# Kernel optimization log

Hardware: AMD Instinct MI355X
Metric: run time of the kernel (lower is better)

## Reference

```python
import jax, jax.numpy as jnp
import numpy as np

# --- static config (from init_kwargs) ---
PC_RANGE = np.array([-51.2, -51.2, -5.0, 51.2, 51.2, 3.0], np.float32)
VOXEL_SIZE = np.array([0.2, 0.2, 8.0], np.float32)
GRID = np.round((PC_RANGE[3:] - PC_RANGE[:3]) / VOXEL_SIZE).astype(np.int64)  # [512,512,1]
GX, GY, GZ = int(GRID[0]), int(GRID[1]), int(GRID[2])
GTOT = GX * GY * GZ  # sentinel linear id for invalid points
MAXV = 30000   # max_voxels_num
MAXP = 20      # max_points_in_voxel
NORM_DIMS = np.array([0, 1, 2], np.int32)
B, N, C = 4, 300000, 5


def _voxelize_one(pts):
    """Hard voxelization of one point cloud [N, C] -> (feat [MAXV,MAXP,C], coors [MAXV,3] (zyx), npts [MAXV])."""
    pc_min = jnp.asarray(PC_RANGE[:3], pts.dtype)
    vsize = jnp.asarray(VOXEL_SIZE, pts.dtype)
    coords = jnp.floor((pts[:, :3] - pc_min) / vsize).astype(jnp.int32)  # [N,3] xyz
    grid = jnp.array([GX, GY, GZ], jnp.int32)
    inb = jnp.all((coords >= 0) & (coords < grid), axis=1)
    lin = coords[:, 2] * (GY * GX) + coords[:, 1] * GX + coords[:, 0]
    lin = jnp.where(inb, lin, GTOT)  # invalid points sort to the end
    order = jnp.argsort(lin)  # stable sort -> deterministic assignment
    lin_s, pts_s, coords_s = lin[order], pts[order], coords[order]
    n = pts.shape[0]
    new = jnp.concatenate([jnp.ones((1,), bool), lin_s[1:] != lin_s[:-1]])
    slot = jnp.cumsum(new.astype(jnp.int32)) - 1           # voxel slot (order of first appearance)
    idx = jnp.arange(n, dtype=jnp.int32)
    run_start = jax.lax.cummax(jnp.where(new, idx, 0))     # start index of each voxel run
    rank = idx - run_start                                  # point rank inside its voxel
    keep = (lin_s < GTOT) & (slot < MAXV) & (rank < MAXP)
    slot_s = jnp.where(keep, slot, MAXV)                    # out-of-range -> dropped by scatter
    rank_s = jnp.where(keep, rank, 0)
    feat = jnp.zeros((MAXV, MAXP, pts.shape[1]), pts.dtype).at[slot_s, rank_s].set(pts_s, mode='drop')
    coors = jnp.full((MAXV, 3), -1, jnp.int32).at[slot_s].set(coords_s[:, ::-1], mode='drop')  # zyx
    npts = jnp.zeros((MAXV,), jnp.int32).at[slot_s].add(keep.astype(jnp.int32), mode='drop')
    return feat, coors, npts


def setup_inputs() -> dict:
    key = jax.random.key(0)
    k1, _ = jax.random.split(key)
    u = jax.random.uniform(k1, (B, N, C), dtype=jnp.float32)
    lo = jnp.array([-51.2, -51.2, -5.0, 0.0, 0.0], jnp.float32)
    hi = jnp.array([51.2, 51.2, 3.0, 1.0, 1.0], jnp.float32)
    points = lo + u * (hi - lo)
    norm_range = jnp.asarray(PC_RANGE)
    return {"points": points, "norm_range": norm_range}


def reference(points, norm_range):
    bs = points.shape[0]
    feat, coors, npts = jax.vmap(_voxelize_one)(points)
    feat = feat.reshape(bs * MAXV, MAXP, C)
    npts = npts.reshape(bs * MAXV)
    bidx = jnp.repeat(jnp.arange(bs, dtype=jnp.int32), MAXV)[:, None]
    coors_batch = jnp.concatenate([bidx, coors.reshape(bs * MAXV, 3)], axis=1)  # [B*MAXV, 4]
    # per-dim range normalization: (f - start) / (max - min) on NORM_DIMS only
    dims = jnp.asarray(NORM_DIMS)
    half = norm_range.shape[0] // 2
    start = jnp.zeros((C,), feat.dtype).at[dims].set(norm_range[:half])
    scale = jnp.ones((C,), feat.dtype).at[dims].set(norm_range[half:] - norm_range[:half])
    f = (feat - start) / scale
    # padding-indicator mask
    mask = (jnp.arange(MAXP)[None, :] < npts[:, None]).astype(f.dtype)
    f = f * mask[:, :, None]
    # unsqueeze(0).permute(0, 3, 2, 1) -> [1, C, MAXP, B*MAXV]
    features = jnp.transpose(f[None], (0, 3, 2, 1))
    return features, coors_batch
```

## Files before the change

### kernel.cpp

```cpp
#include <hip/hip_runtime.h>
#include <stdint.h>

typedef unsigned long long u64;
typedef uint32_t u32;
typedef unsigned char u8;

#define B_ 4
#define N_ 300000
#define C_ 5
#define GX_ 512
#define GY_ 512
#define GZ_ 1
#define GTOT_ (GX_*GY_*GZ_)
#define NW_ (GTOT_/64)
#define MAXV_ 30000
#define MAXP_ 20
#define ROWS_ (B_*MAXV_)
#define OUT0_ELEMS_ (C_*MAXP_*ROWS_)

#define OCCF_Q_ (B_*GTOT_/16)
#define CNT2_Q_ (ROWS_/4)
#define INIT_Q_ (OCCF_Q_ + CNT2_Q_)

__device__ __forceinline__ int voxel_lin(float x, float y, float z) {
    float qx = (x + 51.2f) * 5.0f;
    float qy = (y + 51.2f) * 5.0f;
    float qz = (z + 5.0f) * 0.125f;
    int cx = (int)floorf(qx);
    int cy = (int)floorf(qy);
    int cz = (int)floorf(qz);
    if (cx < 0 || cx >= GX_ || cy < 0 || cy >= GY_ || cz < 0 || cz >= GZ_) return -1;
    return (cz * GY_ + cy) * GX_ + cx;
}

__global__ void k_init(uint4* __restrict__ occF4, uint4* __restrict__ cnt2q) {
    int i = blockIdx.x * blockDim.x + threadIdx.x;
    if (i < OCCF_Q_) occF4[i] = make_uint4(0u, 0u, 0u, 0u);
    else if (i < INIT_Q_) cnt2q[i - OCCF_Q_] = make_uint4(0u, 0u, 0u, 0u);
}

__global__ void k_mark(const float* __restrict__ pts, u8* __restrict__ occF,
                       int* __restrict__ linb) {
    int i = blockIdx.x * blockDim.x + threadIdx.x;
    int b = blockIdx.y;
    if (i >= N_) return;
    const float* p = pts + ((size_t)b * N_ + i) * C_;
    int lin = voxel_lin(p[0], p[1], p[2]);
    linb[(size_t)b * N_ + i] = lin;
    if (lin >= 0) occF[(size_t)b * GTOT_ + lin] = (u8)1;
}

__global__ void k_maskcnt(const u8* __restrict__ occF, u64* __restrict__ occ,
                          u32* __restrict__ wordPop) {
    int i = blockIdx.x * blockDim.x + threadIdx.x;
    int b = blockIdx.y;
    u8 f = occF[(size_t)b * GTOT_ + i];
    u64 m = __ballot(f != 0);
    if ((threadIdx.x & 63) == 0) {
        int w = i >> 6;
        occ[(size_t)b * NW_ + w] = m;
        wordPop[(size_t)b * NW_ + w] = (u32)__popcll(m);
    }
}

__global__ __launch_bounds__(1024) void k_scan2(const u32* __restrict__ wordPop,
                                                u32* __restrict__ wordOff,
                                                u32* __restrict__ nOcc) {
    int b = blockIdx.x;
    int t = threadIdx.x;
    const uint4* wp = (const uint4*)(wordPop + (size_t)b * NW_);
    uint4 v = wp[t];
    __shared__ u32 sh[1024];
    sh[t] = v.x + v.y + v.z + v.w;
    __syncthreads();
    for (int off = 1; off < 1024; off <<= 1) {
        u32 u = (t >= off) ? sh[t - off] : 0u;
        __syncthreads();
        sh[t] += u;
        __syncthreads();
    }
    u32 excl = (t > 0) ? sh[t - 1] : 0u;
    u32* wo = wordOff + (size_t)b * NW_ + t * 4;
    wo[0] = excl;
    wo[1] = excl + v.x;
    wo[2] = excl + v.x + v.y;
    wo[3] = excl + v.x + v.y + v.z;
    if (t == 1023) nOcc[b] = sh[1023];
}

__global__ void k_scatter(const int* __restrict__ linb, const u64* __restrict__ occ,
                          const u32* __restrict__ wordOff,
                          u32* __restrict__ cnt2, u32* __restrict__ idxbuf,
                          u32* __restrict__ voxOf) {
    int i = blockIdx.x * blockDim.x + threadIdx.x;
    int b = blockIdx.y;
    if (i >= N_) return;
    int lin = linb[(size_t)b * N_ + i];
    if (lin < 0) return;
    int w = lin >> 6, bit = lin & 63;
    u32 baseOff = wordOff[(size_t)b * NW_ + w];
    if (baseOff >= MAXV_) return;
    u64 m = occ[(size_t)b * NW_ + w];
    u32 slot = baseOff + (u32)__popcll(m & ((1ull << bit) - 1ull));
    if (slot >= MAXV_) return;
    u32 r = atomicAdd(&cnt2[b * MAXV_ + slot], 1u);
    if (r == 0) voxOf[b * MAXV_ + slot] = (u32)lin;
    if (r < MAXP_) idxbuf[((size_t)b * MAXV_ + slot) * MAXP_ + r] = (u32)i;
}

__global__ void k_out(const float* __restrict__ pts, const float* __restrict__ nr,
                      const u32* __restrict__ voxOf, const u32* __restrict__ cnt2,
                      const u32* __restrict__ idxbuf, const u32* __restrict__ nOcc,
                      float* __restrict__ out0, float* __restrict__ out1) {
    int row = blockIdx.x * blockDim.x + threadIdx.x;
    if (row >= ROWS_) return;
    int b = row / MAXV_;
    int local = row - b * MAXV_;
    u32 nv = nOcc[b];
    bool valid = (u32)local < (nv < MAXV_ ? nv : (u32)MAXV_);
    u32 lin = 0;
    int n = 0;
    u32 idxs[MAXP_];
    if (valid) {
        lin = voxOf[row];
        n = (int)min(cnt2[row], (u32)MAXP_);
        for (int r = 0; r < n; ++r) idxs[r] = idxbuf[(size_t)row * MAXP_ + r];
        for (int a = 1; a < n; ++a) {
            u32 key = idxs[a];
            int j = a - 1;
            while (j >= 0 && idxs[j] > key) { idxs[j + 1] = idxs[j]; --j; }
            idxs[j + 1] = key;
        }
    }
    float4 cr;
    cr.x = (float)b;
    if (valid) {
        int x = lin & (GX_ - 1);
        int y = (lin >> 9) & (GY_ - 1);
        int z = (int)(lin >> 18);
        cr.y = (float)z; cr.z = (float)y; cr.w = (float)x;
    } else {
        cr.y = -1.0f; cr.z = -1.0f; cr.w = -1.0f;
    }
    *(float4*)(out1 + (size_t)row * 4) = cr;
    float s0 = nr[0], s1 = nr[1], s2 = nr[2];
    float d0 = nr[3] - nr[0], d1 = nr[4] - nr[1], d2 = nr[5] - nr[2];
    for (int p = 0; p < MAXP_; ++p) {
        float f0 = 0.f, f1 = 0.f, f2 = 0.f, f3 = 0.f, f4 = 0.f;
        if (p < n) {
            const float* pp = pts + ((size_t)b * N_ + idxs[p]) * C_;
            f0 = (pp[0] - s0) / d0;
            f1 = (pp[1] - s1) / d1;
            f2 = (pp[2] - s2) / d2;
            f3 = pp[3];
            f4 = pp[4];
        }
        out0[(0 * MAXP_ + p) * ROWS_ + row] = f0;
        out0[(1 * MAXP_ + p) * ROWS_ + row] = f1;
        out0[(2 * MAXP_ + p) * ROWS_ + row] = f2;
        out0[(3 * MAXP_ + p) * ROWS_ + row] = f3;
        out0[(4 * MAXP_ + p) * ROWS_ + row] = f4;
    }
}

extern "C" void kernel_launch(void* const* d_in, const int* in_sizes, int n_in,
                              void* d_out, int out_size, void* d_ws, size_t ws_size,
                              hipStream_t stream) {
    const float* pts = (const float*)d_in[0];
    const float* nr  = (const float*)d_in[1];
    float* out0 = (float*)d_out;
    float* out1 = out0 + (size_t)OUT0_ELEMS_;

    uint8_t* ws = (uint8_t*)d_ws;
    u64* occ     = (u64*)(ws + 0);
    u32* wordOff = (u32*)(ws + 131072);
    u32* voxOf   = (u32*)(ws + 196608);
    u32* cnt2    = (u32*)(ws + 676608);
    u32* idxbuf  = (u32*)(ws + 1156608);
    int* linb    = (int*)(ws + 10756608);
    u32* wordPop = (u32*)(ws + 15556608);
    u32* nOcc    = (u32*)(ws + 15622144);
    u8*  occF    = (u8*)(ws + 1156608);

    dim3 gP((N_ + 255) / 256, B_);
    dim3 gV(GTOT_ / 256, B_);
    k_init   <<<(INIT_Q_ + 255) / 256, 256, 0, stream>>>((uint4*)occF, (uint4*)cnt2);
    k_mark   <<<gP, 256, 0, stream>>>(pts, occF, linb);
    k_maskcnt<<<gV, 256, 0, stream>>>(occF, occ, wordPop);
    k_scan2  <<<B_, 1024, 0, stream>>>(wordPop, wordOff, nOcc);
    k_scatter<<<gP, 256, 0, stream>>>(linb, occ, wordOff, cnt2, idxbuf, voxOf);
    k_out    <<<(ROWS_ + 255) / 256, 256, 0, stream>>>(pts, nr, voxOf, cnt2, idxbuf, nOcc, out0, out1);
}
```

Measured before the change: 56.35 us.

## Pack occupancy mask, popcount and offset into one word table; shuffle-based scan

Occupancy bitmask, per-word popcount and exclusive offset are combined into a single uint4 table, so the scatter kernel does one 16-byte load per point instead of two separate loads. The block scan now uses wave shuffles plus a 16-entry shared scan instead of a 10-step shared-memory Hillis-Steele loop full of barriers. Zeroing of the per-voxel counters moves from the init kernel into the mask kernel. This cuts global traffic and synchronisation in the small serial stages, at the cost of a larger table and strided 16-byte reads in the scan.

```diff
diff --git a/kernel.cpp b/kernel.cpp
--- a/kernel.cpp
+++ b/kernel.cpp
@@ -18,10 +18,6 @@
 #define ROWS_ (B_*MAXV_)
 #define OUT0_ELEMS_ (C_*MAXP_*ROWS_)
 
-#define OCCF_Q_ (B_*GTOT_/16)
-#define CNT2_Q_ (ROWS_/4)
-#define INIT_Q_ (OCCF_Q_ + CNT2_Q_)
-
 __device__ __forceinline__ int voxel_lin(float x, float y, float z) {
     float qx = (x + 51.2f) * 5.0f;
     float qy = (y + 51.2f) * 5.0f;
@@ -33,10 +29,9 @@
     return (cz * GY_ + cy) * GX_ + cx;
 }
 
-__global__ void k_init(uint4* __restrict__ occF4, uint4* __restrict__ cnt2q) {
-    int i = blockIdx.x * blockDim.x + threadIdx.x;
-    if (i < OCCF_Q_) occF4[i] = make_uint4(0u, 0u, 0u, 0u);
-    else if (i < INIT_Q_) cnt2q[i - OCCF_Q_] = make_uint4(0u, 0u, 0u, 0u);
+__global__ void k_init(uint4* __restrict__ occF4) {
+    int i = blockIdx.x * blockDim.x + threadIdx.x;
+    occF4[i] = make_uint4(0u, 0u, 0u, 0u);
 }
 
 __global__ void k_mark(const float* __restrict__ pts, u8* __restrict__ occF,
@@ -50,46 +45,59 @@
     if (lin >= 0) occF[(size_t)b * GTOT_ + lin] = (u8)1;
 }
 
-__global__ void k_maskcnt(const u8* __restrict__ occF, u64* __restrict__ occ,
-                          u32* __restrict__ wordPop) {
+__global__ void k_maskcnt(const u8* __restrict__ occF, uint4* __restrict__ wordTab,
+                          u32* __restrict__ cnt2) {
     int i = blockIdx.x * blockDim.x + threadIdx.x;
     int b = blockIdx.y;
     u8 f = occF[(size_t)b * GTOT_ + i];
     u64 m = __ballot(f != 0);
     if ((threadIdx.x & 63) == 0) {
         int w = i >> 6;
-        occ[(size_t)b * NW_ + w] = m;
-        wordPop[(size_t)b * NW_ + w] = (u32)__popcll(m);
-    }
-}
-
-__global__ __launch_bounds__(1024) void k_scan2(const u32* __restrict__ wordPop,
-                                                u32* __restrict__ wordOff,
+        wordTab[(size_t)b * NW_ + w] =
+            make_uint4((u32)m, (u32)(m >> 32), (u32)__popcll(m), 0u);
+    }
+    int g = (blockIdx.y * gridDim.x + blockIdx.x) * blockDim.x + threadIdx.x;
+    if (g < ROWS_) cnt2[g] = 0u;
+}
+
+__global__ __launch_bounds__(1024) void k_scan2(uint4* __restrict__ wordTab,
                                                 u32* __restrict__ nOcc) {
     int b = blockIdx.x;
     int t = threadIdx.x;
-    const uint4* wp = (const uint4*)(wordPop + (size_t)b * NW_);
-    uint4 v = wp[t];
-    __shared__ u32 sh[1024];
-    sh[t] = v.x + v.y + v.z + v.w;
+    uint4* wt = wordTab + (size_t)b * NW_;
+    uint4 q0 = wt[t * 4 + 0], q1 = wt[t * 4 + 1], q2 = wt[t * 4 + 2], q3 = wt[t * 4 + 3];
+    u32 c0 = q0.z, c1 = q1.z, c2 = q2.z, c3 = q3.z;
+    u32 tot = c0 + c1 + c2 + c3;
+    u32 lane = t & 63, wv = t >> 6;
+    u32 s = tot;
+    #pragma unroll
+    for (int d = 1; d < 64; d <<= 1) {
+        u32 u = __shfl_up(s, d, 64);
+        if (lane >= (u32)d) s += u;
+    }
+    __shared__ u32 wsum[16];
+    if (lane == 63) wsum[wv] = s;
     __syncthreads();
-    for (int off = 1; off < 1024; off <<= 1) {
-        u32 u = (t >= off) ? sh[t - off] : 0u;
-        __syncthreads();
-        sh[t] += u;
-        __syncthreads();
-    }
-    u32 excl = (t > 0) ? sh[t - 1] : 0u;
-    u32* wo = wordOff + (size_t)b * NW_ + t * 4;
-    wo[0] = excl;
-    wo[1] = excl + v.x;
-    wo[2] = excl + v.x + v.y;
-    wo[3] = excl + v.x + v.y + v.z;
-    if (t == 1023) nOcc[b] = sh[1023];
-}
-
-__global__ void k_scatter(const int* __restrict__ linb, const u64* __restrict__ occ,
-                          const u32* __restrict__ wordOff,
+    if (t < 16) {
+        u32 ws2 = wsum[t];
+        #pragma unroll
+        for (int d = 1; d < 16; d <<= 1) {
+            u32 u = __shfl_up(ws2, d, 16);
+            if (t >= d) ws2 += u;
+        }
+        wsum[t] = ws2;
+    }
+    __syncthreads();
+    u32 excl = ((wv > 0) ? wsum[wv - 1] : 0u) + (s - tot);
+    u32* base = (u32*)wt;
+    base[(t * 4 + 0) * 4 + 3] = excl;
+    base[(t * 4 + 1) * 4 + 3] = excl + c0;
+    base[(t * 4 + 2) * 4 + 3] = excl + c0 + c1;
+    base[(t * 4 + 3) * 4 + 3] = excl + c0 + c1 + c2;
+    if (t == 1023) nOcc[b] = wsum[15];
+}
+
+__global__ void k_scatter(const int* __restrict__ linb, const uint4* __restrict__ wordTab,
                           u32* __restrict__ cnt2, u32* __restrict__ idxbuf,
                           u32* __restrict__ voxOf) {
     int i = blockIdx.x * blockDim.x + threadIdx.x;
@@ -98,10 +106,11 @@
     int lin = linb[(size_t)b * N_ + i];
     if (lin < 0) return;
     int w = lin >> 6, bit = lin & 63;
-    u32 baseOff = wordOff[(size_t)b * NW_ + w];
-    if (baseOff >= MAXV_) return;
-    u64 m = occ[(size_t)b * NW_ + w];
-    u32 slot = baseOff + (u32)__popcll(m & ((1ull << bit) - 1ull));
+    uint4 q = wordTab[(size_t)b * NW_ + w];
+    u32 off = q.w;
+    if (off >= MAXV_) return;
+    u64 m = (u64)q.x | ((u64)q.y << 32);
+    u32 slot = off + (u32)__popcll(m & ((1ull << bit) - 1ull));
     if (slot >= MAXV_) return;
     u32 r = atomicAdd(&cnt2[b * MAXV_ + slot], 1u);
     if (r == 0) voxOf[b * MAXV_ + slot] = (u32)lin;
@@ -172,22 +181,20 @@
     float* out1 = out0 + (size_t)OUT0_ELEMS_;
 
     uint8_t* ws = (uint8_t*)d_ws;
-    u64* occ     = (u64*)(ws + 0);
-    u32* wordOff = (u32*)(ws + 131072);
-    u32* voxOf   = (u32*)(ws + 196608);
-    u32* cnt2    = (u32*)(ws + 676608);
-    u32* idxbuf  = (u32*)(ws + 1156608);
-    int* linb    = (int*)(ws + 10756608);
-    u32* wordPop = (u32*)(ws + 15556608);
-    u32* nOcc    = (u32*)(ws + 15622144);
-    u8*  occF    = (u8*)(ws + 1156608);
+    uint4* wordTab = (uint4*)(ws + 0);
+    u32* voxOf     = (u32*)(ws + 262144);
+    u32* cnt2      = (u32*)(ws + 742144);
+    u32* idxbuf    = (u32*)(ws + 1222144);
+    int* linb      = (int*)(ws + 10822144);
+    u32* nOcc      = (u32*)(ws + 15622144);
+    u8*  occF      = (u8*)(ws + 1222144);
 
     dim3 gP((N_ + 255) / 256, B_);
     dim3 gV(GTOT_ / 256, B_);
-    k_init   <<<(INIT_Q_ + 255) / 256, 256, 0, stream>>>((uint4*)occF, (uint4*)cnt2);
+    k_init   <<<(B_ * GTOT_ / 16 + 255) / 256, 256, 0, stream>>>((uint4*)occF);
     k_mark   <<<gP, 256, 0, stream>>>(pts, occF, linb);
-    k_maskcnt<<<gV, 256, 0, stream>>>(occF, occ, wordPop);
-    k_scan2  <<<B_, 1024, 0, stream>>>(wordPop, wordOff, nOcc);
-    k_scatter<<<gP, 256, 0, stream>>>(linb, occ, wordOff, cnt2, idxbuf, voxOf);
+    k_maskcnt<<<gV, 256, 0, stream>>>(occF, wordTab, cnt2);
+    k_scan2  <<<B_, 1024, 0, stream>>>(wordTab, nOcc);
+    k_scatter<<<gP, 256, 0, stream>>>(linb, wordTab, cnt2, idxbuf, voxOf);
     k_out    <<<(ROWS_ + 255) / 256, 256, 0, stream>>>(pts, nr, voxOf, cnt2, idxbuf, nOcc, out0, out1);
 }
```

Result: slower. 59.64 us (+5.8%).
